# Kernel optimization log

Hardware: AMD Instinct MI355X
Metric: run time of the kernel (lower is better)

Reference implementation:

```python
import jax, jax.numpy as jnp
import numpy as np

DIM = 128
B, NQ, NK = 4, 4096, 4096
SCALE = DIM ** -0.5


def setup_inputs() -> dict:
    key = jax.random.key(0)
    ks = jax.random.split(key, 13)
    def lin(k, shape, scale=0.02):
        return jax.random.normal(k, shape, dtype=jnp.float32) * scale
    return {
        "query": jax.random.normal(ks[0], (B, NQ, DIM), dtype=jnp.float32),
        "key": jax.random.normal(ks[1], (B, NK, DIM), dtype=jnp.float32),
        "value": jax.random.normal(ks[2], (B, NK, DIM), dtype=jnp.float32),
        "att_bias": jax.random.normal(ks[3], (B, NK), dtype=jnp.float32),
        # params, [in, out] layout (torch Linear is x @ W.T + b)
        "q_w": lin(ks[4], (DIM, DIM)), "q_b": jnp.zeros((DIM,), jnp.float32),
        "k_w": lin(ks[5], (DIM, DIM)),
        "v_w": lin(ks[6], (DIM, DIM)), "v_b": jnp.zeros((DIM,), jnp.float32),
        "vs_w": lin(ks[7], (DIM, 1)), "vs_b": jnp.zeros((1,), jnp.float32),
        "p_w": lin(ks[8], (DIM, DIM)), "p_b": jnp.zeros((DIM,), jnp.float32),
    }


def reference(query, key, value, att_bias, q_w, q_b, k_w, v_w, v_b, vs_w, vs_b, p_w, p_b):
    # projections
    q = query @ q_w + q_b                      # [B, NQ, D]
    k = key @ k_w                              # [B, NK, D] (no bias)
    v = value @ v_w + v_b                      # [B, NK, D]
    # per-key semantic scalar, broadcast over queries: [B, 1, NK]
    semantic = (value @ vs_w + vs_b).reshape(value.shape[0], 1, value.shape[1])
    # scores + biases
    attn = jnp.einsum('bqd,bkd->bqk', q, k) * SCALE + semantic
    attn = attn + att_bias[:, None, :]
    attn = jax.nn.softmax(attn, axis=-1)
    out = jnp.einsum('bqk,bkd->bqd', attn, v)  # [B, NQ, D]
    out = out @ p_w + p_b
    return out
```

## Files before the change

### kernel.cpp

```cpp
#include <hip/hip_runtime.h>

typedef __bf16 bf16x8 __attribute__((ext_vector_type(8)));
typedef float f32x4 __attribute__((ext_vector_type(4)));

#define MFMA16(a,b,c) __builtin_amdgcn_mfma_f32_16x16x32_bf16(a,b,c,0,0,0)

static __device__ __forceinline__ unsigned short f2bf(float f){
  union{float f;unsigned u;}v; v.f=f;
  unsigned u=v.u;
  u += 0x7fffu + ((u>>16)&1u);
  return (unsigned short)(u>>16);
}
static __device__ __forceinline__ float bf2f(unsigned short h){
  union{unsigned u;float f;}v; v.u=((unsigned)h)<<16; return v.f;
}
static __device__ __forceinline__ unsigned cvtpk(float lo, float hi){
  unsigned r;
  asm("v_cvt_pk_bf16_f32 %0, %1, %2" : "=v"(r) : "v"(lo), "v"(hi));
  return r;
}
static __device__ __forceinline__ void gload16(const void* g, void* l){
  __builtin_amdgcn_global_load_lds(
    (const __attribute__((address_space(1))) unsigned int*)(uintptr_t)g,
    (__attribute__((address_space(3))) unsigned int*)(uintptr_t)l,
    16, 0, 0);
}

#define SCALE_QK 0.08838834764831845f
#define LOG2E    1.44269504088896340f
#define THR_L2   11.541560327111708f

#define SWZ128(r,c) (((r)<<7) + ((c) ^ (((r)&7)<<3)))


__global__ __launch_bounds__(256) void k_proj(
    const float* __restrict__ query, const float* __restrict__ key,
    const float* __restrict__ value, const float* __restrict__ att_bias,
    const float* __restrict__ q_w, const float* __restrict__ q_b,
    const float* __restrict__ k_w, const float* __restrict__ v_w,
    const float* __restrict__ v_b, const float* __restrict__ vs_w,
    const float* __restrict__ vs_b,
    unsigned short* __restrict__ qp, unsigned short* __restrict__ kp,
    unsigned short* __restrict__ vpt, float* __restrict__ biasc)
{
  const int t = blockIdx.y;
  const float* X = (t==0) ? query : ((t==1) ? key : value);
  const float* W = (t==0) ? q_w  : ((t==1) ? k_w : v_w);
  const int tid = threadIdx.x;
  const int row0 = blockIdx.x * 64;

  __shared__ __align__(16) unsigned short Wt[128][136];
  __shared__ __align__(16) unsigned short Xs[64][136];
  __shared__ float vsw_s[128];

  #pragma unroll 4
  for (int i=0;i<16;i++){
    int idx = tid*64 + i*4;
    float4 v4 = *(const float4*)(W + idx);
    Wt[(idx+0)&127][(idx+0)>>7] = f2bf(v4.x);
    Wt[(idx+1)&127][(idx+1)>>7] = f2bf(v4.y);
    Wt[(idx+2)&127][(idx+2)>>7] = f2bf(v4.z);
    Wt[(idx+3)&127][(idx+3)>>7] = f2bf(v4.w);
  }
  {
    const float* Xb = X + (size_t)row0*128;
    #pragma unroll
    for (int i=0;i<8;i++){
      int f4 = i*256 + tid;
      int row = f4>>5, c4 = f4&31;
      float4 v = *(const float4*)(Xb + row*128 + c4*4);
      ushort4 h;
      h.x = f2bf(v.x); h.y = f2bf(v.y); h.z = f2bf(v.z); h.w = f2bf(v.w);
      *(ushort4*)&Xs[row][c4*4] = h;
    }
  }
  if (t==2 && tid<128) vsw_s[tid] = vs_w[tid];
  __syncthreads();

  const int w = tid>>6, lane = tid&63, lr = lane&15, lg = lane>>4;
  f32x4 acc[8];
  #pragma unroll
  for (int nt=0;nt<8;nt++) acc[nt] = (f32x4){0.f,0.f,0.f,0.f};
  #pragma unroll
  for (int kk=0;kk<4;kk++){
    bf16x8 a = *(const bf16x8*)&Xs[w*16+lr][kk*32+lg*8];
    #pragma unroll
    for (int nt=0;nt<8;nt++){
      bf16x8 bb = *(const bf16x8*)&Wt[nt*16+lr][kk*32+lg*8];
      acc[nt] = MFMA16(a,bb,acc[nt]);
    }
  }
  const float* bias = (t==0) ? q_b : ((t==2) ? v_b : (const float*)nullptr);
  const float sc = (t==0) ? (SCALE_QK*LOG2E) : 1.f;
  #pragma unroll
  for (int nt=0;nt<8;nt++){
    int col = nt*16+lr;
    float bv = bias ? bias[col] : 0.f;
    #pragma unroll
    for (int r=0;r<4;r++){
      int row = row0 + w*16 + lg*4 + r;
      unsigned short h = f2bf((acc[nt][r] + bv) * sc);
      if (t==0)      qp[(size_t)row*128+col] = h;
      else if (t==1) kp[(size_t)row*128+col] = h;
      else {
        int bi = row>>12, n = row&4095;
        int k5 = n & 31;
        int pos = 8*((k5>>2)&3) + (k5&3) + 4*(k5>>4);
        int np = (n & ~31) | pos;
        vpt[((size_t)bi*128+col)*4096 + np] = h;
      }
    }
  }
  if (t==2){
    int rl = tid>>2, part = tid&3;
    float s = 0.f;
    #pragma unroll
    for (int j=0;j<32;j++){
      int d = part*32+j;
      s += bf2f(Xs[rl][d]) * vsw_s[d];
    }
    s += __shfl_xor(s,1);
    s += __shfl_xor(s,2);
    if ((tid&3)==0){
      int rg = row0 + rl;
      biasc[rg] = (s + vs_b[0] + att_bias[rg]) * LOG2E;
    }
  }
}

__global__ __launch_bounds__(256,4) void k_flash(
    const unsigned short* __restrict__ qp, const unsigned short* __restrict__ kp,
    const unsigned short* __restrict__ vpt, const float* __restrict__ biasc,
    unsigned short* __restrict__ opart, float* __restrict__ ml)
{
  const int f = blockIdx.x;
  const int xcd = f & 7, slot = f >> 3;
  const int group = xcd*2 + (slot>>6);
  const int b = group>>2, split = group&3;
  const int q0 = (slot & 63) * 64;

  const int tid = threadIdx.x;
  const int w = tid>>6, lane = tid&63;
  const int q15 = lane&15, g = lane>>4;

  __shared__ __align__(16) unsigned short Ks[2][32*128];
  __shared__ __align__(16) unsigned short Vs[2][128*32];
  __shared__ __align__(16) float Bs[1024];

  const unsigned short* kbase = kp  + (size_t)(b*4096 + split*1024)*128;
  const unsigned short* vbase = vpt + (size_t)b*128*4096 + split*1024;
  const float* bbase = biasc + b*4096 + split*1024;

  gload16(bbase + w*256 + lane*4, &Bs[w*256]);
  bf16x8 qf[4];
  {
    const unsigned short* qrow = qp + ((size_t)(b*4096 + q0 + w*16 + q15))*128;
    #pragma unroll
    for (int kk=0;kk<4;kk++) qf[kk] = *(const bf16x8*)(qrow + kk*32 + g*8);
  }

  #define STAGE(bf_, k0_) do{                                                 \
    const char* kb_ = (const char*)kbase + (size_t)(k0_)*256;                 \
    const char* vb_ = (const char*)vbase + (size_t)(k0_)*2;                   \
    _Pragma("unroll")                                                         \
    for (int i=0;i<2;i++){                                                    \
      int s_ = w*2+i;                                                         \
      int kr = s_*4 + (lane>>4);                                              \
      gload16(kb_ + kr*256 + (((lane&15)*16) ^ ((kr&7)*16)),                  \
              (char*)Ks[bf_] + s_*1024);                                      \
      int vd = s_*16 + (lane>>2);                                             \
      gload16(vb_ + (size_t)vd*8192 + (((lane&3) ^ (vd&3))*16),               \
              (char*)Vs[bf_] + s_*1024);                                      \
    }                                                                         \
  }while(0)

  float m_run = -INFINITY, l_run = 0.f;
  f32x4 acc[8];
  #pragma unroll
  for (int nt=0;nt<8;nt++) acc[nt] = (f32x4){0.f,0.f,0.f,0.f};

  STAGE(0, 0);
  __syncthreads();

  const int voff = (q15<<6) + ((g ^ (q15&3))<<4);

  for (int t=0;t<32;t++){
    const int cur = t & 1;
    if (t<31) STAGE(cur^1, (t+1)*32);

    const unsigned short* Kc = Ks[cur];
    const char* Vc = (const char*)Vs[cur];

    f32x4 s0 = {}, s1 = {};
    __builtin_amdgcn_s_setprio(1);
    #pragma unroll
    for (int kk=0;kk<4;kk++){
      bf16x8 a0 = *(const bf16x8*)&Kc[SWZ128(q15,      kk*32 + g*8)];
      bf16x8 a1 = *(const bf16x8*)&Kc[SWZ128(16 + q15, kk*32 + g*8)];
      s0 = MFMA16(a0, qf[kk], s0);
      s1 = MFMA16(a1, qf[kk], s1);
    }
    __builtin_amdgcn_s_setprio(0);

    const float* Bt = &Bs[t*32];
    float4 b0 = *(const float4*)&Bt[g*4];
    float4 b1 = *(const float4*)&Bt[16 + g*4];
    float tmax = -1e30f;
    #pragma unroll
    for (int c=0;c<4;c++){
      s0[c] += ((const float*)&b0)[c];
      s1[c] += ((const float*)&b1)[c];
      tmax = fmaxf(tmax, fmaxf(s0[c], s1[c]));
    }
    tmax = fmaxf(tmax, __shfl_xor(tmax, 16));
    tmax = fmaxf(tmax, __shfl_xor(tmax, 32));

    if (!__all(tmax <= m_run + THR_L2)){
      float mn = fmaxf(m_run, tmax);
      float corr = __builtin_exp2f(m_run - mn);
      m_run = mn;
      l_run *= corr;
      float c0 = __shfl(corr, g*4+0);
      float c1 = __shfl(corr, g*4+1);
      float c2 = __shfl(corr, g*4+2);
      float c3 = __shfl(corr, g*4+3);
      #pragma unroll
      for (int nt=0;nt<8;nt++){
        acc[nt][0]*=c0; acc[nt][1]*=c1; acc[nt][2]*=c2; acc[nt][3]*=c3;
      }
    }

    float rs = 0.f;
    #pragma unroll
    for (int c=0;c<4;c++){
      s0[c] = __builtin_exp2f(s0[c]-m_run); rs += s0[c];
      s1[c] = __builtin_exp2f(s1[c]-m_run); rs += s1[c];
    }
    rs += __shfl_xor(rs, 16);
    rs += __shfl_xor(rs, 32);
    l_run += rs;

    union { unsigned u[4]; bf16x8 v; } pu;
    pu.u[0] = cvtpk(s0[0], s0[1]);
    pu.u[1] = cvtpk(s0[2], s0[3]);
    pu.u[2] = cvtpk(s1[0], s1[1]);
    pu.u[3] = cvtpk(s1[2], s1[3]);

    __builtin_amdgcn_s_setprio(1);
    #pragma unroll
    for (int nt=0;nt<8;nt++){
      bf16x8 vf = *(const bf16x8*)(Vc + voff + nt*1024);
      acc[nt] = MFMA16(pu.v, vf, acc[nt]);
    }
    __builtin_amdgcn_s_setprio(0);

    __syncthreads();
  }
  #undef STAGE

  const size_t rowbase = (size_t)split*16384 + (size_t)b*4096 + q0;
  float i0 = 1.f/__shfl(l_run, g*4+0);
  float i1 = 1.f/__shfl(l_run, g*4+1);
  float i2 = 1.f/__shfl(l_run, g*4+2);
  float i3 = 1.f/__shfl(l_run, g*4+3);
  #pragma unroll
  for (int nt=0;nt<8;nt++){
    int col = nt*16 + q15;
    size_t rb = rowbase + w*16 + g*4;
    opart[(rb+0)*128 + col] = f2bf(acc[nt][0]*i0);
    opart[(rb+1)*128 + col] = f2bf(acc[nt][1]*i1);
    opart[(rb+2)*128 + col] = f2bf(acc[nt][2]*i2);
    opart[(rb+3)*128 + col] = f2bf(acc[nt][3]*i3);
  }
  if (lane < 16){
    size_t rg = rowbase + w*16 + lane;
    ml[rg*2]   = m_run;
    ml[rg*2+1] = l_run;
  }
}

__global__ __launch_bounds__(256) void k_outproj(
    const unsigned short* __restrict__ opart, const float* __restrict__ ml,
    const float* __restrict__ p_w, const float* __restrict__ p_b,
    float* __restrict__ out)
{
  const int tid = threadIdx.x;
  const int row0 = blockIdx.x*64;
  __shared__ __align__(16) unsigned short Wt[128][136];
  __shared__ __align__(16) unsigned short Xs[64][136];
  __shared__ float wmg[4][64];

  #pragma unroll 4
  for (int i=0;i<16;i++){
    int idx = tid*64 + i*4;
    float4 v4 = *(const float4*)(p_w + idx);
    Wt[(idx+0)&127][(idx+0)>>7] = f2bf(v4.x);
    Wt[(idx+1)&127][(idx+1)>>7] = f2bf(v4.y);
    Wt[(idx+2)&127][(idx+2)>>7] = f2bf(v4.z);
    Wt[(idx+3)&127][(idx+3)>>7] = f2bf(v4.w);
  }
  if (tid < 64){
    int row = row0 + tid;
    float m[4], l[4];
    #pragma unroll
    for (int i=0;i<4;i++){
      m[i] = ml[((size_t)i*16384 + row)*2];
      l[i] = ml[((size_t)i*16384 + row)*2 + 1];
    }
    float M = fmaxf(fmaxf(m[0],m[1]),fmaxf(m[2],m[3]));
    float wi[4], wsum = 0.f;
    #pragma unroll
    for (int i=0;i<4;i++){ wi[i] = __builtin_exp2f(m[i]-M)*l[i]; wsum += wi[i]; }
    float inv = 1.f/wsum;
    #pragma unroll
    for (int i=0;i<4;i++) wmg[i][tid] = wi[i]*inv;
  }
  __syncthreads();
  #pragma unroll
  for (int i=0;i<4;i++){
    int e = tid*32 + i*8;
    int row = e>>7, col = e&127;
    float a8[8];
    #pragma unroll
    for (int j=0;j<8;j++) a8[j] = 0.f;
    #pragma unroll
    for (int s=0;s<4;s++){
      uint4 v = *(const uint4*)(opart + ((size_t)s*16384 + row0 + row)*128 + col);
      float wv = wmg[s][row];
      const unsigned short* hp = (const unsigned short*)&v;
      #pragma unroll
      for (int j=0;j<8;j++) a8[j] += wv * bf2f(hp[j]);
    }
    unsigned short h8[8];
    #pragma unroll
    for (int j=0;j<8;j++) h8[j] = f2bf(a8[j]);
    *(uint4*)&Xs[row][col] = *(const uint4*)h8;
  }
  __syncthreads();

  const int w=tid>>6, lane=tid&63, lr=lane&15, lg=lane>>4;
  f32x4 acc[8];
  #pragma unroll
  for (int nt=0;nt<8;nt++) acc[nt] = (f32x4){0.f,0.f,0.f,0.f};
  #pragma unroll
  for (int kk=0;kk<4;kk++){
    bf16x8 a = *(const bf16x8*)&Xs[w*16+lr][kk*32+lg*8];
    #pragma unroll
    for (int nt=0;nt<8;nt++){
      bf16x8 bb = *(const bf16x8*)&Wt[nt*16+lr][kk*32+lg*8];
      acc[nt] = MFMA16(a,bb,acc[nt]);
    }
  }
  #pragma unroll
  for (int nt=0;nt<8;nt++){
    int col = nt*16+lr;
    float pb = p_b[col];
    #pragma unroll
    for (int r=0;r<4;r++){
      int row = row0 + w*16 + lg*4 + r;
      out[(size_t)row*128+col] = acc[nt][r] + pb;
    }
  }
}

extern "C" void kernel_launch(void* const* d_in, const int* in_sizes, int n_in,
                              void* d_out, int out_size, void* d_ws, size_t ws_size,
                              hipStream_t stream) {
  (void)in_sizes; (void)n_in; (void)out_size; (void)ws_size;
  const float* query    = (const float*)d_in[0];
  const float* key      = (const float*)d_in[1];
  const float* value    = (const float*)d_in[2];
  const float* att_bias = (const float*)d_in[3];
  const float* q_w = (const float*)d_in[4];
  const float* q_b = (const float*)d_in[5];
  const float* k_w = (const float*)d_in[6];
  const float* v_w = (const float*)d_in[7];
  const float* v_b = (const float*)d_in[8];
  const float* vs_w = (const float*)d_in[9];
  const float* vs_b = (const float*)d_in[10];
  const float* p_w = (const float*)d_in[11];
  const float* p_b = (const float*)d_in[12];

  char* ws = (char*)d_ws;
  unsigned short* qp    = (unsigned short*)(ws);
  unsigned short* kp    = (unsigned short*)(ws + 4194304);
  unsigned short* vpt   = (unsigned short*)(ws + 8388608);
  float*          biasc = (float*)(ws + 12582912);
  unsigned short* opart = (unsigned short*)(ws + 12648448);
  float*          ml    = (float*)(ws + 29425664);

  hipLaunchKernelGGL(k_proj, dim3(256,3), dim3(256), 0, stream,
    query,key,value,att_bias,q_w,q_b,k_w,v_w,v_b,vs_w,vs_b,qp,kp,vpt,biasc);
  hipLaunchKernelGGL(k_flash, dim3(1024), dim3(256), 0, stream,
    qp,kp,vpt,biasc,opart,ml);
  hipLaunchKernelGGL(k_outproj, dim3(256), dim3(256), 0, stream,
    opart,ml,p_w,p_b,(float*)d_out);
}
```

Before: 88.20 us.

## Split KV eight ways, stage V transpose and output through LDS

The flash kernel's key split grows from 4 to 8 partitions, doubling the grid to 2048 blocks with 512 keys each, and the merge kernel now combines 8 partials over 32-row tiles. The transposed V write in the projection kernel is staged through LDS, and the output projection also goes through LDS, so both global writes become coalesced 16-byte stores. The LDS bias staging in the flash kernel is dropped in favour of direct global float4 loads. This adds more occupancy and parallel work at the cost of twice the partial-output traffic and a larger merge.

```diff
diff --git a/kernel.cpp b/kernel.cpp
--- a/kernel.cpp
+++ b/kernel.cpp
@@ -90,41 +90,60 @@
       acc[nt] = MFMA16(a,bb,acc[nt]);
     }
   }
-  const float* bias = (t==0) ? q_b : ((t==2) ? v_b : (const float*)nullptr);
-  const float sc = (t==0) ? (SCALE_QK*LOG2E) : 1.f;
-  #pragma unroll
-  for (int nt=0;nt<8;nt++){
-    int col = nt*16+lr;
-    float bv = bias ? bias[col] : 0.f;
-    #pragma unroll
-    for (int r=0;r<4;r++){
-      int row = row0 + w*16 + lg*4 + r;
-      unsigned short h = f2bf((acc[nt][r] + bv) * sc);
-      if (t==0)      qp[(size_t)row*128+col] = h;
-      else if (t==1) kp[(size_t)row*128+col] = h;
-      else {
-        int bi = row>>12, n = row&4095;
-        int k5 = n & 31;
+
+  if (t < 2){
+    const float* bias = (t==0) ? q_b : (const float*)nullptr;
+    const float sc = (t==0) ? (SCALE_QK*LOG2E) : 1.f;
+    unsigned short* dstm = (t==0) ? qp : kp;
+    #pragma unroll
+    for (int nt=0;nt<8;nt++){
+      int col = nt*16+lr;
+      float bv = bias ? bias[col] : 0.f;
+      #pragma unroll
+      for (int r=0;r<4;r++){
+        int row = row0 + w*16 + lg*4 + r;
+        dstm[(size_t)row*128+col] = f2bf((acc[nt][r] + bv) * sc);
+      }
+    }
+  } else {
+    {
+      int rl = tid>>2, part = tid&3;
+      float s = 0.f;
+      #pragma unroll
+      for (int j=0;j<32;j++){
+        int d = part*32+j;
+        s += bf2f(Xs[rl][d]) * vsw_s[d];
+      }
+      s += __shfl_xor(s,1);
+      s += __shfl_xor(s,2);
+      if ((tid&3)==0){
+        int rg = row0 + rl;
+        biasc[rg] = (s + vs_b[0] + att_bias[rg]) * LOG2E;
+      }
+    }
+    __syncthreads();
+    unsigned short* Vls = (unsigned short*)Wt;
+    #pragma unroll
+    for (int nt=0;nt<8;nt++){
+      int col = nt*16+lr;
+      float bv = v_b[col];
+      #pragma unroll
+      for (int r=0;r<4;r++){
+        int rl_ = w*16 + lg*4 + r;
+        int k5 = rl_ & 31;
         int pos = 8*((k5>>2)&3) + (k5&3) + 4*(k5>>4);
-        int np = (n & ~31) | pos;
-        vpt[((size_t)bi*128+col)*4096 + np] = h;
+        int np = (rl_ & 32) | pos;
+        Vls[col*72 + np] = f2bf(acc[nt][r] + bv);
       }
     }
-  }
-  if (t==2){
-    int rl = tid>>2, part = tid&3;
-    float s = 0.f;
-    #pragma unroll
-    for (int j=0;j<32;j++){
-      int d = part*32+j;
-      s += bf2f(Xs[rl][d]) * vsw_s[d];
-    }
-    s += __shfl_xor(s,1);
-    s += __shfl_xor(s,2);
-    if ((tid&3)==0){
-      int rg = row0 + rl;
-      biasc[rg] = (s + vs_b[0] + att_bias[rg]) * LOG2E;
-    }
+    __syncthreads();
+    int d = tid>>1, half = tid&1;
+    int bi = row0>>12, n0 = row0&4095;
+    unsigned short* dst = vpt + ((size_t)(bi*128+d))*4096 + n0 + half*32;
+    const unsigned short* src = Vls + d*72 + half*32;
+    #pragma unroll
+    for (int i=0;i<4;i++)
+      *(uint4*)(dst + i*8) = *(const uint4*)(src + i*8);
   }
 }
 
@@ -135,8 +154,8 @@
 {
   const int f = blockIdx.x;
   const int xcd = f & 7, slot = f >> 3;
-  const int group = xcd*2 + (slot>>6);
-  const int b = group>>2, split = group&3;
+  const int group = xcd*4 + (slot>>6);
+  const int b = group>>3, split = group&7;
   const int q0 = (slot & 63) * 64;
 
   const int tid = threadIdx.x;
@@ -145,13 +164,11 @@
 
   __shared__ __align__(16) unsigned short Ks[2][32*128];
   __shared__ __align__(16) unsigned short Vs[2][128*32];
-  __shared__ __align__(16) float Bs[1024];
-
-  const unsigned short* kbase = kp  + (size_t)(b*4096 + split*1024)*128;
-  const unsigned short* vbase = vpt + (size_t)b*128*4096 + split*1024;
-  const float* bbase = biasc + b*4096 + split*1024;
-
-  gload16(bbase + w*256 + lane*4, &Bs[w*256]);
+
+  const unsigned short* kbase = kp  + (size_t)(b*4096 + split*512)*128;
+  const unsigned short* vbase = vpt + (size_t)b*128*4096 + split*512;
+  const float* bbase = biasc + b*4096 + split*512;
+
   bf16x8 qf[4];
   {
     const unsigned short* qrow = qp + ((size_t)(b*4096 + q0 + w*16 + q15))*128;
@@ -184,9 +201,13 @@
 
   const int voff = (q15<<6) + ((g ^ (q15&3))<<4);
 
-  for (int t=0;t<32;t++){
+  for (int t=0;t<16;t++){
     const int cur = t & 1;
-    if (t<31) STAGE(cur^1, (t+1)*32);
+    if (t<15) STAGE(cur^1, (t+1)*32);
+
+    const float* Bt = bbase + t*32;
+    float4 b0 = *(const float4*)(Bt + g*4);
+    float4 b1 = *(const float4*)(Bt + 16 + g*4);
 
     const unsigned short* Kc = Ks[cur];
     const char* Vc = (const char*)Vs[cur];
@@ -202,9 +223,6 @@
     }
     __builtin_amdgcn_s_setprio(0);
 
-    const float* Bt = &Bs[t*32];
-    float4 b0 = *(const float4*)&Bt[g*4];
-    float4 b1 = *(const float4*)&Bt[16 + g*4];
     float tmax = -1e30f;
     #pragma unroll
     for (int c=0;c<4;c++){
@@ -285,10 +303,10 @@
     float* __restrict__ out)
 {
   const int tid = threadIdx.x;
-  const int row0 = blockIdx.x*64;
+  const int row0 = blockIdx.x*32;
   __shared__ __align__(16) unsigned short Wt[128][136];
-  __shared__ __align__(16) unsigned short Xs[64][136];
-  __shared__ float wmg[4][64];
+  __shared__ __align__(16) unsigned short Xs[32][136];
+  __shared__ float wmg[8][32];
 
   #pragma unroll 4
   for (int i=0;i<16;i++){
@@ -299,32 +317,34 @@
     Wt[(idx+2)&127][(idx+2)>>7] = f2bf(v4.z);
     Wt[(idx+3)&127][(idx+3)>>7] = f2bf(v4.w);
   }
-  if (tid < 64){
+  if (tid < 32){
     int row = row0 + tid;
-    float m[4], l[4];
-    #pragma unroll
-    for (int i=0;i<4;i++){
+    float m[8], l[8];
+    #pragma unroll
+    for (int i=0;i<8;i++){
       m[i] = ml[((size_t)i*16384 + row)*2];
       l[i] = ml[((size_t)i*16384 + row)*2 + 1];
     }
-    float M = fmaxf(fmaxf(m[0],m[1]),fmaxf(m[2],m[3]));
-    float wi[4], wsum = 0.f;
-    #pragma unroll
-    for (int i=0;i<4;i++){ wi[i] = __builtin_exp2f(m[i]-M)*l[i]; wsum += wi[i]; }
+    float M = m[0];
+    #pragma unroll
+    for (int i=1;i<8;i++) M = fmaxf(M, m[i]);
+    float wi[8], wsum = 0.f;
+    #pragma unroll
+    for (int i=0;i<8;i++){ wi[i] = __builtin_exp2f(m[i]-M)*l[i]; wsum += wi[i]; }
     float inv = 1.f/wsum;
     #pragma unroll
-    for (int i=0;i<4;i++) wmg[i][tid] = wi[i]*inv;
-  }
-  __syncthreads();
-  #pragma unroll
-  for (int i=0;i<4;i++){
-    int e = tid*32 + i*8;
+    for (int i=0;i<8;i++) wmg[i][tid] = wi[i]*inv;
+  }
+  __syncthreads();
+  #pragma unroll
+  for (int i=0;i<2;i++){
+    int e = (i*256 + tid)*8;
     int row = e>>7, col = e&127;
     float a8[8];
     #pragma unroll
     for (int j=0;j<8;j++) a8[j] = 0.f;
     #pragma unroll
-    for (int s=0;s<4;s++){
+    for (int s=0;s<8;s++){
       uint4 v = *(const uint4*)(opart + ((size_t)s*16384 + row0 + row)*128 + col);
       float wv = wmg[s][row];
       const unsigned short* hp = (const unsigned short*)&v;
@@ -339,27 +359,39 @@
   __syncthreads();
 
   const int w=tid>>6, lane=tid&63, lr=lane&15, lg=lane>>4;
-  f32x4 acc[8];
-  #pragma unroll
-  for (int nt=0;nt<8;nt++) acc[nt] = (f32x4){0.f,0.f,0.f,0.f};
+  const int r0 = (w&1)*16, c0 = (w>>1)*64;
+  f32x4 acc[4];
+  #pragma unroll
+  for (int nt=0;nt<4;nt++) acc[nt] = (f32x4){0.f,0.f,0.f,0.f};
   #pragma unroll
   for (int kk=0;kk<4;kk++){
-    bf16x8 a = *(const bf16x8*)&Xs[w*16+lr][kk*32+lg*8];
-    #pragma unroll
-    for (int nt=0;nt<8;nt++){
-      bf16x8 bb = *(const bf16x8*)&Wt[nt*16+lr][kk*32+lg*8];
+    bf16x8 a = *(const bf16x8*)&Xs[r0+lr][kk*32+lg*8];
+    #pragma unroll
+    for (int nt=0;nt<4;nt++){
+      bf16x8 bb = *(const bf16x8*)&Wt[c0+nt*16+lr][kk*32+lg*8];
       acc[nt] = MFMA16(a,bb,acc[nt]);
     }
   }
-  #pragma unroll
-  for (int nt=0;nt<8;nt++){
-    int col = nt*16+lr;
+  __syncthreads();
+  float* Os = (float*)Wt;
+  #pragma unroll
+  for (int nt=0;nt<4;nt++){
+    int col = c0 + nt*16 + lr;
     float pb = p_b[col];
     #pragma unroll
     for (int r=0;r<4;r++){
-      int row = row0 + w*16 + lg*4 + r;
-      out[(size_t)row*128+col] = acc[nt][r] + pb;
-    }
+      int row = r0 + lg*4 + r;
+      Os[row*132 + col] = acc[nt][r] + pb;
+    }
+  }
+  __syncthreads();
+  {
+    int row = tid>>3, seg = tid&7;
+    const float* src = Os + row*132 + seg*16;
+    float* dst = out + (size_t)(row0+row)*128 + seg*16;
+    #pragma unroll
+    for (int i=0;i<4;i++)
+      *(float4*)(dst + i*4) = *(const float4*)(src + i*4);
   }
 }
 
@@ -387,12 +419,12 @@
   unsigned short* vpt   = (unsigned short*)(ws + 8388608);
   float*          biasc = (float*)(ws + 12582912);
   unsigned short* opart = (unsigned short*)(ws + 12648448);
-  float*          ml    = (float*)(ws + 29425664);
+  float*          ml    = (float*)(ws + 46202880);
 
   hipLaunchKernelGGL(k_proj, dim3(256,3), dim3(256), 0, stream,
     query,key,value,att_bias,q_w,q_b,k_w,v_w,v_b,vs_w,vs_b,qp,kp,vpt,biasc);
-  hipLaunchKernelGGL(k_flash, dim3(1024), dim3(256), 0, stream,
+  hipLaunchKernelGGL(k_flash, dim3(2048), dim3(256), 0, stream,
     qp,kp,vpt,biasc,opart,ml);
-  hipLaunchKernelGGL(k_outproj, dim3(256), dim3(256), 0, stream,
+  hipLaunchKernelGGL(k_outproj, dim3(512), dim3(256), 0, stream,
     opart,ml,p_w,p_b,(float*)d_out);
 }
```

Measured after the change: 90.34 us. 2.4% more time.
